# Optimization experiments

Measured on AMD Instinct MI355X. Metric: run time of the kernel, lower is better.

## Reference

```python
import jax, jax.numpy as jnp
import numpy as np

VOCAB = 100000
EMBED = 64
HIDDEN = 256
SEQ = 200
BATCH = 4096


def setup_inputs() -> dict:
    key = jax.random.key(0)
    ks = jax.random.split(key, 12)
    s = 0.02
    return {
        "user_hist": jax.random.randint(ks[0], (BATCH, SEQ), 0, VOCAB),
        "target_item": jax.random.randint(ks[1], (BATCH,), 0, VOCAB),
        "user_emb": jax.random.normal(ks[2], (VOCAB, EMBED), jnp.float32) * s,
        "item_emb": jax.random.normal(ks[3], (VOCAB, EMBED), jnp.float32) * s,
        "attn_w1": jax.random.normal(ks[4], (4 * EMBED, HIDDEN), jnp.float32) * s,
        "attn_b1": jnp.zeros((HIDDEN,), jnp.float32),
        "attn_w2": jax.random.normal(ks[5], (HIDDEN, 1), jnp.float32) * s,
        "attn_b2": jnp.zeros((1,), jnp.float32),
        "mlp_w1": jax.random.normal(ks[6], (2 * EMBED, HIDDEN), jnp.float32) * s,
        "mlp_b1": jnp.zeros((HIDDEN,), jnp.float32),
        "mlp_w2": jax.random.normal(ks[7], (HIDDEN, 1), jnp.float32) * s,
        "mlp_b2": jnp.zeros((1,), jnp.float32),
    }


def reference(user_hist, target_item, user_emb, item_emb,
              attn_w1, attn_b1, attn_w2, attn_b2,
              mlp_w1, mlp_b1, mlp_w2, mlp_b2):
    # [B, S, E] history embeddings, [B, 1, E] target embedding
    h = user_emb[user_hist]
    t = item_emb[target_item][:, None, :]
    tb = jnp.broadcast_to(t, h.shape)
    # attention MLP over [B, S, 4E]
    att_in = jnp.concatenate([h, tb, h - t, h * t], axis=-1)
    att_h = jax.nn.relu(att_in @ attn_w1 + attn_b1)
    att_logits = (att_h @ attn_w2 + attn_b2)[..., 0]            # [B, S]
    att_w = jax.nn.softmax(att_logits, axis=-1)[..., None]      # [B, S, 1]
    user_interest = jnp.sum(h * att_w, axis=1)                  # [B, E]
    # prediction head on [B, 2E]
    mlp_in = jnp.concatenate([user_interest, t[:, 0, :]], axis=-1)
    mlp_h = jax.nn.relu(mlp_in @ mlp_w1 + mlp_b1)
    out = jax.nn.sigmoid(mlp_h @ mlp_w2 + mlp_b2)               # [B, 1]
    return out
```

## Files before the change

kernel.cpp:

```cpp
#include <hip/hip_runtime.h>
#include <math.h>

#define EMBED   64
#define HIDDEN  256
#define SEQ     200
#define SEQP    208
#define MT      13
#define VOCAB   100000

typedef _Float16 f16x8  __attribute__((ext_vector_type(8)));
typedef float    f32x4  __attribute__((ext_vector_type(4)));
typedef float    f32x2  __attribute__((ext_vector_type(2)));

__global__ void din_precompute(const float* __restrict__ attn_w1,
                               const float* __restrict__ mlp_w1,
                               uint2* __restrict__ fragB8,
                               _Float16* __restrict__ fragW3,
                               _Float16* __restrict__ fragDt,
                               _Float16* __restrict__ fragB2) {
  const int gid = blockIdx.x * 256 + threadIdx.x;
  if (gid < 2048) {
    const int i = gid >> 7, rem = gid & 127, kc = rem >> 6, lane = rem & 63;
    const int n = i * 16 + (lane & 15);
    const int kb = kc * 32 + (lane >> 4) * 8;
    float v[8];
    #pragma unroll
    for (int j = 0; j < 8; ++j)
      v[j] = 16.0f * (attn_w1[(kb + j) * HIDDEN + n] + attn_w1[(128 + kb + j) * HIDDEN + n]);
    int lo = __builtin_amdgcn_cvt_pk_fp8_f32(v[0], v[1], 0, false);
    lo     = __builtin_amdgcn_cvt_pk_fp8_f32(v[2], v[3], lo, true);
    int hi = __builtin_amdgcn_cvt_pk_fp8_f32(v[4], v[5], 0, false);
    hi     = __builtin_amdgcn_cvt_pk_fp8_f32(v[6], v[7], hi, true);
    fragB8[gid] = uint2{(unsigned)lo, (unsigned)hi};
  } else if (gid < 4096) {
    const int g = gid - 2048;
    const int i = g >> 7, rem = g & 127, kc = rem >> 6, lane = rem & 63;
    const int n = i * 16 + (lane & 15);
    const int kb = kc * 32 + (lane >> 4) * 8;
    #pragma unroll
    for (int j = 0; j < 8; ++j)
      fragW3[g * 8 + j] = (_Float16)(16.0f * attn_w1[(192 + kb + j) * HIDDEN + n]);
  } else if (gid < 6144) {
    const int g = gid - 4096;
    const int i = g >> 7, rem = g & 127, kc = rem >> 6, lane = rem & 63;
    const int n = i * 16 + (lane & 15);
    const int kb = kc * 32 + (lane >> 4) * 8;
    #pragma unroll
    for (int j = 0; j < 8; ++j)
      fragDt[g * 8 + j] = (_Float16)(attn_w1[(64 + kb + j) * HIDDEN + n]
                                   - attn_w1[(128 + kb + j) * HIDDEN + n]);
  } else {
    const int g = gid - 6144;
    const int nt = g >> 8, kc = (g >> 6) & 3, lane = g & 63;
    const int n = nt * 16 + (lane & 15);
    const int kb = kc * 32 + (lane >> 4) * 8;
    #pragma unroll
    for (int j = 0; j < 8; ++j)
      fragB2[g * 8 + j] = (_Float16)mlp_w1[(kb + j) * HIDDEN + n];
  }
}

__global__ void din_emb8(const float* __restrict__ user_emb, unsigned char* __restrict__ emb8) {
  const int g = blockIdx.x * 256 + threadIdx.x;
  const int base = g * 8;
  const float4 x = *reinterpret_cast<const float4*>(&user_emb[base]);
  const float4 y = *reinterpret_cast<const float4*>(&user_emb[base + 4]);
  int lo = __builtin_amdgcn_cvt_pk_fp8_f32(16.f * x.x, 16.f * x.y, 0, false);
  lo     = __builtin_amdgcn_cvt_pk_fp8_f32(16.f * x.z, 16.f * x.w, lo, true);
  int hi = __builtin_amdgcn_cvt_pk_fp8_f32(16.f * y.x, 16.f * y.y, 0, false);
  hi     = __builtin_amdgcn_cvt_pk_fp8_f32(16.f * y.z, 16.f * y.w, hi, true);
  *reinterpret_cast<uint2*>(&emb8[base]) = uint2{(unsigned)lo, (unsigned)hi};
}

__global__ __launch_bounds__(512, 8)
void din_fused_kernel(const int* __restrict__ user_hist,
                      const int* __restrict__ target_item,
                      const float* __restrict__ user_emb,
                      const float* __restrict__ item_emb,
                      const float* __restrict__ attn_b1,
                      const float* __restrict__ attn_w2,
                      const float* __restrict__ mlp_b1,
                      const float* __restrict__ mlp_w2,
                      const float* __restrict__ mlp_b2,
                      const uint2* __restrict__ fragB8,
                      const _Float16* __restrict__ fragW3,
                      const _Float16* __restrict__ fragDt,
                      const _Float16* __restrict__ fragB2,
                      const unsigned char* __restrict__ emb8,
                      float* __restrict__ out)
{
  __shared__ __align__(16) uint2 Hf8[MT * 2 * 64];
  __shared__ __align__(16) _Float16 t16[EMBED];
  __shared__ int   histL[SEQP];
  __shared__ float lp[8][SEQP];
  __shared__ float weights[SEQP];
  __shared__ __align__(16) _Float16 mi16[EMBED];
  __shared__ float red[16];

  const int b    = blockIdx.x;
  const int tid  = threadIdx.x;
  const int lane = tid & 63;
  const int wave = tid >> 6;
  const int m    = lane & 15;
  const int quad = lane >> 4;

  if (tid < EMBED) t16[tid] = (_Float16)item_emb[target_item[b] * EMBED + tid];
  if (tid < SEQP) histL[tid] = (tid < SEQ) ? user_hist[b * SEQ + tid] : 0;

  long long Aw8[2][2];
  #pragma unroll
  for (int i = 0; i < 2; ++i)
    #pragma unroll
    for (int c = 0; c < 2; ++c)
      Aw8[i][c] = __builtin_bit_cast(long long, fragB8[((2 * wave + i) * 2 + c) * 64 + lane]);
  __syncthreads();

  if (emb8) {
    for (int slot = tid; slot < MT * 2 * 64; slot += 512) {
      const int ln = slot & 63, kcomb = slot >> 6;
      const int st = kcomb >> 1, kc = kcomb & 1;
      const int s = st * 16 + (ln & 15);
      const int kb = kc * 32 + (ln >> 4) * 8;
      uint2 pv = uint2{0u, 0u};
      if (s < SEQ)
        pv = *reinterpret_cast<const uint2*>(&emb8[histL[s] * EMBED + kb]);
      Hf8[slot] = pv;
    }
  } else {
    for (int slot = tid; slot < MT * 2 * 64; slot += 512) {
      const int ln = slot & 63, kcomb = slot >> 6;
      const int st = kcomb >> 1, kc = kcomb & 1;
      const int s = st * 16 + (ln & 15);
      const int kb = kc * 32 + (ln >> 4) * 8;
      uint2 pv = uint2{0u, 0u};
      if (s < SEQ) {
        const float4* src = reinterpret_cast<const float4*>(&user_emb[histL[s] * EMBED + kb]);
        const float4 x = src[0], y = src[1];
        int lo = __builtin_amdgcn_cvt_pk_fp8_f32(16.f * x.x, 16.f * x.y, 0, false);
        lo     = __builtin_amdgcn_cvt_pk_fp8_f32(16.f * x.z, 16.f * x.w, lo, true);
        int hi = __builtin_amdgcn_cvt_pk_fp8_f32(16.f * y.x, 16.f * y.y, 0, false);
        hi     = __builtin_amdgcn_cvt_pk_fp8_f32(16.f * y.z, 16.f * y.w, hi, true);
        pv = uint2{(unsigned)lo, (unsigned)hi};
      }
      Hf8[slot] = pv;
    }
  }

  const f16x8 tv0 = *reinterpret_cast<const f16x8*>(&t16[quad * 8]);
  const f16x8 tv1 = *reinterpret_cast<const f16x8*>(&t16[32 + quad * 8]);

  long long AwT[2][2];
  #pragma unroll
  for (int i = 0; i < 2; ++i) {
    #pragma unroll
    for (int c = 0; c < 2; ++c) {
      const f16x8 w3v = reinterpret_cast<const f16x8*>(fragW3)[((2 * wave + i) * 2 + c) * 64 + lane];
      const f16x8 p = w3v * (c ? tv1 : tv0);
      int lo = __builtin_amdgcn_cvt_pk_fp8_f32((float)p[0], (float)p[1], 0, false);
      lo     = __builtin_amdgcn_cvt_pk_fp8_f32((float)p[2], (float)p[3], lo, true);
      int hi = __builtin_amdgcn_cvt_pk_fp8_f32((float)p[4], (float)p[5], 0, false);
      hi     = __builtin_amdgcn_cvt_pk_fp8_f32((float)p[6], (float)p[7], hi, true);
      AwT[i][c] = __builtin_bit_cast(long long, uint2{(unsigned)lo, (unsigned)hi});
    }
  }

  float cn[2][4], w2n[2][4];
  #pragma unroll
  for (int i = 0; i < 2; ++i) {
    const int tile = 2 * wave + i;
    const f16x8 d0 = reinterpret_cast<const f16x8*>(fragDt)[(tile * 2 + 0) * 64 + lane];
    const f16x8 d1 = reinterpret_cast<const f16x8*>(fragDt)[(tile * 2 + 1) * 64 + lane];
    f32x4 acc = {0.f, 0.f, 0.f, 0.f};
    acc = __builtin_amdgcn_mfma_f32_16x16x32_f16(d0, tv0, acc, 0, 0, 0);
    acc = __builtin_amdgcn_mfma_f32_16x16x32_f16(d1, tv1, acc, 0, 0, 0);
    const int nb = tile * 16 + quad * 4;
    const float4 b1v = *reinterpret_cast<const float4*>(&attn_b1[nb]);
    const float4 w2v = *reinterpret_cast<const float4*>(&attn_w2[nb]);
    cn[i][0] = 256.0f * (b1v.x + acc[0]);
    cn[i][1] = 256.0f * (b1v.y + acc[1]);
    cn[i][2] = 256.0f * (b1v.z + acc[2]);
    cn[i][3] = 256.0f * (b1v.w + acc[3]);
    w2n[i][0] = w2v.x * (1.0f / 256.0f);
    w2n[i][1] = w2v.y * (1.0f / 256.0f);
    w2n[i][2] = w2v.z * (1.0f / 256.0f);
    w2n[i][3] = w2v.w * (1.0f / 256.0f);
  }
  __syncthreads();

  #pragma unroll 2
  for (int st = 0; st < MT; ++st) {
    const long long b0 = __builtin_bit_cast(long long, Hf8[(st * 2 + 0) * 64 + lane]);
    const long long b1 = __builtin_bit_cast(long long, Hf8[(st * 2 + 1) * 64 + lane]);
    float lg = 0.f;
    #pragma unroll
    for (int i = 0; i < 2; ++i) {
      f32x4 acc = {cn[i][0], cn[i][1], cn[i][2], cn[i][3]};
      acc = __builtin_amdgcn_mfma_f32_16x16x32_fp8_fp8(Aw8[i][0], b0, acc, 0, 0, 0);
      acc = __builtin_amdgcn_mfma_f32_16x16x32_fp8_fp8(Aw8[i][1], b1, acc, 0, 0, 0);
      acc = __builtin_amdgcn_mfma_f32_16x16x32_fp8_fp8(AwT[i][0], b0, acc, 0, 0, 0);
      acc = __builtin_amdgcn_mfma_f32_16x16x32_fp8_fp8(AwT[i][1], b1, acc, 0, 0, 0);
      #pragma unroll
      for (int r = 0; r < 4; ++r)
        lg += fmaxf(acc[r], 0.0f) * w2n[i][r];
    }
    lg += __shfl_xor(lg, 16, 64);
    lg += __shfl_xor(lg, 32, 64);
    if (lane < 16) lp[wave][st * 16 + lane] = lg;
  }
  __syncthreads();

  float v = -INFINITY, e = 0.0f;
  if (wave < 4) {
    if (tid < SEQ)
      v = lp[0][tid] + lp[1][tid] + lp[2][tid] + lp[3][tid]
        + lp[4][tid] + lp[5][tid] + lp[6][tid] + lp[7][tid];
    float mx = v;
    #pragma unroll
    for (int off = 32; off; off >>= 1) mx = fmaxf(mx, __shfl_xor(mx, off, 64));
    if (lane == 0) red[wave] = mx;
  }
  __syncthreads();
  if (wave < 4) {
    const float mx = fmaxf(fmaxf(red[0], red[1]), fmaxf(red[2], red[3]));
    e = (tid < SEQ) ? expf(v - mx) : 0.0f;
    float ssum = e;
    #pragma unroll
    for (int off = 32; off; off >>= 1) ssum += __shfl_xor(ssum, off, 64);
    if (lane == 0) red[4 + wave] = ssum;
  }
  __syncthreads();
  if (wave < 4) {
    const float tot = red[4] + red[5] + red[6] + red[7];
    if (tid < SEQP) weights[tid] = (tid < SEQ) ? e / tot : 0.0f;
  }
  __syncthreads();

  {
    const int kc = wave & 1, g = wave >> 1;
    float pk[8];
    #pragma unroll
    for (int j = 0; j < 8; ++j) pk[j] = 0.f;
    #pragma unroll
    for (int st2 = 0; st2 < 4; ++st2) {
      const int st = g + st2 * 4;
      if (st < MT) {
        const float wt = weights[st * 16 + m];
        const uint2 hv = Hf8[(st * 2 + kc) * 64 + lane];
        const f32x2 f0 = __builtin_amdgcn_cvt_pk_f32_fp8((int)hv.x, false);
        const f32x2 f1 = __builtin_amdgcn_cvt_pk_f32_fp8((int)hv.x, true);
        const f32x2 f2 = __builtin_amdgcn_cvt_pk_f32_fp8((int)hv.y, false);
        const f32x2 f3 = __builtin_amdgcn_cvt_pk_f32_fp8((int)hv.y, true);
        pk[0] += wt * f0.x;  pk[1] += wt * f0.y;
        pk[2] += wt * f1.x;  pk[3] += wt * f1.y;
        pk[4] += wt * f2.x;  pk[5] += wt * f2.y;
        pk[6] += wt * f3.x;  pk[7] += wt * f3.y;
      }
    }
    #pragma unroll
    for (int j = 0; j < 8; ++j) {
      float p = pk[j];
      p += __shfl_xor(p, 1, 64);
      p += __shfl_xor(p, 2, 64);
      p += __shfl_xor(p, 4, 64);
      p += __shfl_xor(p, 8, 64);
      pk[j] = p;
    }
    if (m == 0) {
      #pragma unroll
      for (int j = 0; j < 8; ++j)
        lp[g][kc * 32 + quad * 8 + j] = pk[j];
    }
  }
  __syncthreads();
  if (tid < EMBED)
    mi16[tid] = (_Float16)((lp[0][tid] + lp[1][tid] + lp[2][tid] + lp[3][tid]) * 0.0625f);
  __syncthreads();

  {
    const f16x8 mb0 = *reinterpret_cast<const f16x8*>(&mi16[quad * 8]);
    const f16x8 mb1 = *reinterpret_cast<const f16x8*>(&mi16[32 + quad * 8]);
    float z = 0.f;
    #pragma unroll
    for (int i = 0; i < 2; ++i) {
      const f16x8* B2 = reinterpret_cast<const f16x8*>(fragB2) + ((2 * wave + i) * 4) * 64 + lane;
      const int nb = (2 * wave + i) * 16 + quad * 4;
      const float4 bb = *reinterpret_cast<const float4*>(&mlp_b1[nb]);
      const float4 ww = *reinterpret_cast<const float4*>(&mlp_w2[nb]);
      f32x4 acc = {bb.x, bb.y, bb.z, bb.w};
      acc = __builtin_amdgcn_mfma_f32_16x16x32_f16(B2[0],   mb0, acc, 0, 0, 0);
      acc = __builtin_amdgcn_mfma_f32_16x16x32_f16(B2[64],  mb1, acc, 0, 0, 0);
      acc = __builtin_amdgcn_mfma_f32_16x16x32_f16(B2[128], tv0, acc, 0, 0, 0);
      acc = __builtin_amdgcn_mfma_f32_16x16x32_f16(B2[192], tv1, acc, 0, 0, 0);
      z += fmaxf(acc[0], 0.0f) * ww.x;
      z += fmaxf(acc[1], 0.0f) * ww.y;
      z += fmaxf(acc[2], 0.0f) * ww.z;
      z += fmaxf(acc[3], 0.0f) * ww.w;
    }
    z += __shfl_xor(z, 16, 64);
    z += __shfl_xor(z, 32, 64);
    if (lane == 0) red[wave] = z;
  }
  __syncthreads();
  if (tid == 0) {
    const float zz = red[0] + red[1] + red[2] + red[3]
                   + red[4] + red[5] + red[6] + red[7] + mlp_b2[0];
    out[b] = 1.0f / (1.0f + expf(-zz));
  }
}

extern "C" void kernel_launch(void* const* d_in, const int* in_sizes, int n_in,
                              void* d_out, int out_size, void* d_ws, size_t ws_size,
                              hipStream_t stream) {
  const int*   user_hist   = (const int*)  d_in[0];
  const int*   target_item = (const int*)  d_in[1];
  const float* user_emb    = (const float*)d_in[2];
  const float* item_emb    = (const float*)d_in[3];
  const float* attn_w1     = (const float*)d_in[4];
  const float* attn_b1     = (const float*)d_in[5];
  const float* attn_w2     = (const float*)d_in[6];
  const float* mlp_w1      = (const float*)d_in[8];
  const float* mlp_b1      = (const float*)d_in[9];
  const float* mlp_w2      = (const float*)d_in[10];
  const float* mlp_b2      = (const float*)d_in[11];
  float* out = (float*)d_out;

  uint2*    fragB8 = (uint2*)d_ws;
  _Float16* fragW3 = (_Float16*)((char*)d_ws + 16384);
  _Float16* fragDt = (_Float16*)((char*)d_ws + 49152);
  _Float16* fragB2 = (_Float16*)((char*)d_ws + 81920);
  const size_t emb8_off = 147456;
  const size_t emb8_bytes = (size_t)VOCAB * EMBED;
  unsigned char* emb8 = nullptr;
  if (ws_size >= emb8_off + emb8_bytes)
    emb8 = (unsigned char*)d_ws + emb8_off;

  din_precompute<<<40, 256, 0, stream>>>(attn_w1, mlp_w1, fragB8, fragW3, fragDt, fragB2);
  if (emb8)
    din_emb8<<<(VOCAB * EMBED / 8 + 255) / 256, 256, 0, stream>>>(user_emb, emb8);

  const int batch = in_sizes[1];
  din_fused_kernel<<<batch, 512, 0, stream>>>(
      user_hist, target_item, user_emb, item_emb,
      attn_b1, attn_w2, mlp_b1, mlp_w2, mlp_b2,
      fragB8, fragW3, fragDt, fragB2, emb8, out);
}
```

Measured before the change: 176.0 us.

## Merge setup kernels and pack both K-halves of each history row into one LDS slot

Fuses the weight-fragment precompute and the fp8 embedding-table conversion into a single setup launch, removing one kernel launch and its gap. The shared history tile now holds both 32-byte K-halves of a row in one 16-byte uint4 slot per lane. That halves the number of gather-loop iterations and turns the two LDS reads per MFMA step into one wide read. The cost is that each thread issues two separate 8-byte global loads per slot, and the weighted-sum phase reads a full 16-byte slot but uses only half of it.

```diff
diff --git a/kernel.cpp b/kernel.cpp
--- a/kernel.cpp
+++ b/kernel.cpp
@@ -12,12 +12,16 @@
 typedef float    f32x4  __attribute__((ext_vector_type(4)));
 typedef float    f32x2  __attribute__((ext_vector_type(2)));
 
-__global__ void din_precompute(const float* __restrict__ attn_w1,
-                               const float* __restrict__ mlp_w1,
-                               uint2* __restrict__ fragB8,
-                               _Float16* __restrict__ fragW3,
-                               _Float16* __restrict__ fragDt,
-                               _Float16* __restrict__ fragB2) {
+
+__global__ void din_setup(const float* __restrict__ attn_w1,
+                          const float* __restrict__ mlp_w1,
+                          const float* __restrict__ user_emb,
+                          uint2* __restrict__ fragB8,
+                          _Float16* __restrict__ fragW3,
+                          _Float16* __restrict__ fragDt,
+                          _Float16* __restrict__ fragB2,
+                          unsigned char* __restrict__ emb8,
+                          int do_emb) {
   const int gid = blockIdx.x * 256 + threadIdx.x;
   if (gid < 2048) {
     const int i = gid >> 7, rem = gid & 127, kc = rem >> 6, lane = rem & 63;
@@ -49,7 +53,7 @@
     for (int j = 0; j < 8; ++j)
       fragDt[g * 8 + j] = (_Float16)(attn_w1[(64 + kb + j) * HIDDEN + n]
                                    - attn_w1[(128 + kb + j) * HIDDEN + n]);
-  } else {
+  } else if (gid < 10240) {
     const int g = gid - 6144;
     const int nt = g >> 8, kc = (g >> 6) & 3, lane = g & 63;
     const int n = nt * 16 + (lane & 15);
@@ -57,19 +61,19 @@
     #pragma unroll
     for (int j = 0; j < 8; ++j)
       fragB2[g * 8 + j] = (_Float16)mlp_w1[(kb + j) * HIDDEN + n];
-  }
-}
-
-__global__ void din_emb8(const float* __restrict__ user_emb, unsigned char* __restrict__ emb8) {
-  const int g = blockIdx.x * 256 + threadIdx.x;
-  const int base = g * 8;
-  const float4 x = *reinterpret_cast<const float4*>(&user_emb[base]);
-  const float4 y = *reinterpret_cast<const float4*>(&user_emb[base + 4]);
-  int lo = __builtin_amdgcn_cvt_pk_fp8_f32(16.f * x.x, 16.f * x.y, 0, false);
-  lo     = __builtin_amdgcn_cvt_pk_fp8_f32(16.f * x.z, 16.f * x.w, lo, true);
-  int hi = __builtin_amdgcn_cvt_pk_fp8_f32(16.f * y.x, 16.f * y.y, 0, false);
-  hi     = __builtin_amdgcn_cvt_pk_fp8_f32(16.f * y.z, 16.f * y.w, hi, true);
-  *reinterpret_cast<uint2*>(&emb8[base]) = uint2{(unsigned)lo, (unsigned)hi};
+  } else if (do_emb) {
+    const int g = gid - 10240;
+    if (g < VOCAB * EMBED / 8) {
+      const int base = g * 8;
+      const float4 x = *reinterpret_cast<const float4*>(&user_emb[base]);
+      const float4 y = *reinterpret_cast<const float4*>(&user_emb[base + 4]);
+      int lo = __builtin_amdgcn_cvt_pk_fp8_f32(16.f * x.x, 16.f * x.y, 0, false);
+      lo     = __builtin_amdgcn_cvt_pk_fp8_f32(16.f * x.z, 16.f * x.w, lo, true);
+      int hi = __builtin_amdgcn_cvt_pk_fp8_f32(16.f * y.x, 16.f * y.y, 0, false);
+      hi     = __builtin_amdgcn_cvt_pk_fp8_f32(16.f * y.z, 16.f * y.w, hi, true);
+      *reinterpret_cast<uint2*>(&emb8[base]) = uint2{(unsigned)lo, (unsigned)hi};
+    }
+  }
 }
 
 __global__ __launch_bounds__(512, 8)
@@ -89,7 +93,7 @@
                       const unsigned char* __restrict__ emb8,
                       float* __restrict__ out)
 {
-  __shared__ __align__(16) uint2 Hf8[MT * 2 * 64];
+  __shared__ __align__(16) uint4 Hf8[MT * 64];
   __shared__ __align__(16) _Float16 t16[EMBED];
   __shared__ int   histL[SEQP];
   __shared__ float lp[8][SEQP];
@@ -116,31 +120,40 @@
   __syncthreads();
 
   if (emb8) {
-    for (int slot = tid; slot < MT * 2 * 64; slot += 512) {
-      const int ln = slot & 63, kcomb = slot >> 6;
-      const int st = kcomb >> 1, kc = kcomb & 1;
+    for (int slot = tid; slot < MT * 64; slot += 512) {
+      const int ln = slot & 63, st = slot >> 6;
       const int s = st * 16 + (ln & 15);
-      const int kb = kc * 32 + (ln >> 4) * 8;
-      uint2 pv = uint2{0u, 0u};
-      if (s < SEQ)
-        pv = *reinterpret_cast<const uint2*>(&emb8[histL[s] * EMBED + kb]);
+      const int q = ln >> 4;
+      uint4 pv = uint4{0u, 0u, 0u, 0u};
+      if (s < SEQ) {
+        const unsigned char* row = &emb8[histL[s] * EMBED];
+        const uint2 a = *reinterpret_cast<const uint2*>(row + q * 8);
+        const uint2 c = *reinterpret_cast<const uint2*>(row + 32 + q * 8);
+        pv = uint4{a.x, a.y, c.x, c.y};
+      }
       Hf8[slot] = pv;
     }
   } else {
-    for (int slot = tid; slot < MT * 2 * 64; slot += 512) {
-      const int ln = slot & 63, kcomb = slot >> 6;
-      const int st = kcomb >> 1, kc = kcomb & 1;
+    for (int slot = tid; slot < MT * 64; slot += 512) {
+      const int ln = slot & 63, st = slot >> 6;
       const int s = st * 16 + (ln & 15);
-      const int kb = kc * 32 + (ln >> 4) * 8;
-      uint2 pv = uint2{0u, 0u};
+      const int q = ln >> 4;
+      uint4 pv = uint4{0u, 0u, 0u, 0u};
       if (s < SEQ) {
-        const float4* src = reinterpret_cast<const float4*>(&user_emb[histL[s] * EMBED + kb]);
-        const float4 x = src[0], y = src[1];
-        int lo = __builtin_amdgcn_cvt_pk_fp8_f32(16.f * x.x, 16.f * x.y, 0, false);
-        lo     = __builtin_amdgcn_cvt_pk_fp8_f32(16.f * x.z, 16.f * x.w, lo, true);
-        int hi = __builtin_amdgcn_cvt_pk_fp8_f32(16.f * y.x, 16.f * y.y, 0, false);
-        hi     = __builtin_amdgcn_cvt_pk_fp8_f32(16.f * y.z, 16.f * y.w, hi, true);
-        pv = uint2{(unsigned)lo, (unsigned)hi};
+        const float* row = &user_emb[histL[s] * EMBED];
+        const float4 x0 = *reinterpret_cast<const float4*>(row + q * 8);
+        const float4 y0 = *reinterpret_cast<const float4*>(row + q * 8 + 4);
+        const float4 x1 = *reinterpret_cast<const float4*>(row + 32 + q * 8);
+        const float4 y1 = *reinterpret_cast<const float4*>(row + 32 + q * 8 + 4);
+        int a0 = __builtin_amdgcn_cvt_pk_fp8_f32(16.f * x0.x, 16.f * x0.y, 0, false);
+        a0     = __builtin_amdgcn_cvt_pk_fp8_f32(16.f * x0.z, 16.f * x0.w, a0, true);
+        int a1 = __builtin_amdgcn_cvt_pk_fp8_f32(16.f * y0.x, 16.f * y0.y, 0, false);
+        a1     = __builtin_amdgcn_cvt_pk_fp8_f32(16.f * y0.z, 16.f * y0.w, a1, true);
+        int c0 = __builtin_amdgcn_cvt_pk_fp8_f32(16.f * x1.x, 16.f * x1.y, 0, false);
+        c0     = __builtin_amdgcn_cvt_pk_fp8_f32(16.f * x1.z, 16.f * x1.w, c0, true);
+        int c1 = __builtin_amdgcn_cvt_pk_fp8_f32(16.f * y1.x, 16.f * y1.y, 0, false);
+        c1     = __builtin_amdgcn_cvt_pk_fp8_f32(16.f * y1.z, 16.f * y1.w, c1, true);
+        pv = uint4{(unsigned)a0, (unsigned)a1, (unsigned)c0, (unsigned)c1};
       }
       Hf8[slot] = pv;
     }
@@ -189,8 +202,9 @@
 
   #pragma unroll 2
   for (int st = 0; st < MT; ++st) {
-    const long long b0 = __builtin_bit_cast(long long, Hf8[(st * 2 + 0) * 64 + lane]);
-    const long long b1 = __builtin_bit_cast(long long, Hf8[(st * 2 + 1) * 64 + lane]);
+    const uint4 hv = Hf8[st * 64 + lane];
+    const long long b0 = __builtin_bit_cast(long long, uint2{hv.x, hv.y});
+    const long long b1 = __builtin_bit_cast(long long, uint2{hv.z, hv.w});
     float lg = 0.f;
     #pragma unroll
     for (int i = 0; i < 2; ++i) {
@@ -245,11 +259,13 @@
       const int st = g + st2 * 4;
       if (st < MT) {
         const float wt = weights[st * 16 + m];
-        const uint2 hv = Hf8[(st * 2 + kc) * 64 + lane];
-        const f32x2 f0 = __builtin_amdgcn_cvt_pk_f32_fp8((int)hv.x, false);
-        const f32x2 f1 = __builtin_amdgcn_cvt_pk_f32_fp8((int)hv.x, true);
-        const f32x2 f2 = __builtin_amdgcn_cvt_pk_f32_fp8((int)hv.y, false);
-        const f32x2 f3 = __builtin_amdgcn_cvt_pk_f32_fp8((int)hv.y, true);
+        const uint4 hq = Hf8[st * 64 + lane];
+        const unsigned lo = kc ? hq.z : hq.x;
+        const unsigned hi = kc ? hq.w : hq.y;
+        const f32x2 f0 = __builtin_amdgcn_cvt_pk_f32_fp8((int)lo, false);
+        const f32x2 f1 = __builtin_amdgcn_cvt_pk_f32_fp8((int)lo, true);
+        const f32x2 f2 = __builtin_amdgcn_cvt_pk_f32_fp8((int)hi, false);
+        const f32x2 f3 = __builtin_amdgcn_cvt_pk_f32_fp8((int)hi, true);
         pk[0] += wt * f0.x;  pk[1] += wt * f0.y;
         pk[2] += wt * f1.x;  pk[3] += wt * f1.y;
         pk[4] += wt * f2.x;  pk[5] += wt * f2.y;
@@ -334,9 +350,10 @@
   if (ws_size >= emb8_off + emb8_bytes)
     emb8 = (unsigned char*)d_ws + emb8_off;
 
-  din_precompute<<<40, 256, 0, stream>>>(attn_w1, mlp_w1, fragB8, fragW3, fragDt, fragB2);
-  if (emb8)
-    din_emb8<<<(VOCAB * EMBED / 8 + 255) / 256, 256, 0, stream>>>(user_emb, emb8);
+  const int setup_gids = 10240 + VOCAB * EMBED / 8;
+  din_setup<<<(setup_gids + 255) / 256, 256, 0, stream>>>(
+      attn_w1, mlp_w1, user_emb, fragB8, fragW3, fragDt, fragB2,
+      emb8 ? emb8 : (unsigned char*)d_ws, emb8 ? 1 : 0);
 
   const int batch = in_sizes[1];
   din_fused_kernel<<<batch, 512, 0, stream>>>(
```

Result: slower. 190.8 us (+8.4%).
